# Performance work log

Hardware: AMD Instinct MI355X
Metric: run time of the kernel (lower is better)

## Reference

```python
import jax, jax.numpy as jnp
import numpy as np


def _maxpool2x2(t):
    # t: [B, C, H, W] -> [B, C, H//2, W//2]
    B, C, H, W = t.shape
    return t.reshape(B, C, H // 2, 2, W // 2, 2).max(axis=(3, 5))


def setup_inputs() -> dict:
    key = jax.random.key(0)
    ks = jax.random.split(key, 6)
    ch = 64
    B, H, W = 16, 64, 64
    x = jax.random.normal(ks[0], (B, ch, H, W), dtype=jnp.float32)
    # 1x1 conv weights (spectral-norm wrapper just rescales weights; use unit-scale weights)
    w_theta = jax.random.normal(ks[1], (ch // 8, ch), dtype=jnp.float32) * 0.05
    w_phi = jax.random.normal(ks[2], (ch // 8, ch), dtype=jnp.float32) * 0.05
    w_g = jax.random.normal(ks[3], (ch // 2, ch), dtype=jnp.float32) * 0.05
    w_o = jax.random.normal(ks[4], (ch, ch // 2), dtype=jnp.float32) * 0.05
    gamma = jnp.float32(0.5)  # nonzero so attention branch contributes
    return {"x": x, "w_theta": w_theta, "w_phi": w_phi, "w_g": w_g, "w_o": w_o, "gamma": gamma}


def reference(x, w_theta, w_phi, w_g, w_o, gamma):
    B, C, H, W = x.shape
    N = H * W
    # 1x1 convs are channel contractions
    theta = jnp.einsum('oc,bchw->bohw', w_theta, x).reshape(B, -1, N)          # [B, C/8, N]
    phi = _maxpool2x2(jnp.einsum('oc,bchw->bohw', w_phi, x)).reshape(B, -1, N // 4)  # [B, C/8, N/4]
    g = _maxpool2x2(jnp.einsum('oc,bchw->bohw', w_g, x)).reshape(B, -1, N // 4)      # [B, C/2, N/4]
    # attention: no scaling (faithful to source)
    scores = jnp.einsum('bdn,bdm->bnm', theta, phi)       # [B, N, N/4]
    beta = jax.nn.softmax(scores, axis=-1)
    o = jnp.einsum('bdm,bnm->bdn', g, beta)               # [B, C/2, N]
    o = o.reshape(B, C // 2, H, W)
    o = jnp.einsum('oc,bchw->bohw', w_o, o)               # [B, C, H, W]
    return gamma * o + x
```

## Files before the change

### kernel.cpp

```cpp
#include <hip/hip_runtime.h>
#include <hip/hip_bf16.h>

#define BB 16
#define CC 64
#define NN 4096
#define MM 1024

typedef unsigned short u16;
typedef __attribute__((ext_vector_type(8))) short bf16x8;
typedef __attribute__((ext_vector_type(4))) float f32x4;

__device__ inline u16 f2bf(float f) {
    union { float f; unsigned u; } v; v.f = f;
    return (u16)((v.u + 0x7FFFu + ((v.u >> 16) & 1u)) >> 16);
}
__device__ inline bf16x8 ld_bf16x8(const u16* p) {
    union { uint4 u; bf16x8 b; } c; c.u = *(const uint4*)p; return c.b;
}


__global__ __launch_bounds__(256) void prep_kernel(
    const float* __restrict__ x, const float* __restrict__ w_theta,
    const float* __restrict__ w_phi, const float* __restrict__ w_g,
    u16* __restrict__ theta_b, u16* __restrict__ phi_b, u16* __restrict__ gT_b)
{
    __shared__ float wT[64 * 48];
    __shared__ float pool[40 * 128];

    const int t = threadIdx.x;
    const int b = blockIdx.y;

    for (int i = t; i < 64 * 8; i += 256)  { int o = i >> 6, c = i & 63; wT[c * 48 + o] = w_theta[i]; }
    for (int i = t; i < 64 * 8; i += 256)  { int o = i >> 6, c = i & 63; wT[c * 48 + 8 + o] = w_phi[i]; }
    for (int i = t; i < 64 * 32; i += 256) { int o = i >> 6, c = i & 63; wT[c * 48 + 16 + o] = w_g[i]; }
    __syncthreads();

    const int p = blockIdx.x * 256 + t;
    const float* xb = x + (size_t)b * CC * NN;

    float xr[64];
    #pragma unroll
    for (int c = 0; c < 64; ++c) xr[c] = xb[c * NN + p];

    float4 acc[12];
    #pragma unroll
    for (int k = 0; k < 12; ++k) acc[k] = make_float4(0.f, 0.f, 0.f, 0.f);

    #pragma unroll
    for (int c = 0; c < 64; ++c) {
        const float xv = xr[c];
        const float4* w4 = (const float4*)&wT[c * 48];
        #pragma unroll
        for (int k = 0; k < 12; ++k) {
            float4 w = w4[k];
            acc[k].x += w.x * xv; acc[k].y += w.y * xv;
            acc[k].z += w.z * xv; acc[k].w += w.w * xv;
        }
    }

    {
        union { u16 s[8]; uint4 v; } tb;
        tb.s[0] = f2bf(acc[0].x); tb.s[1] = f2bf(acc[0].y);
        tb.s[2] = f2bf(acc[0].z); tb.s[3] = f2bf(acc[0].w);
        tb.s[4] = f2bf(acc[1].x); tb.s[5] = f2bf(acc[1].y);
        tb.s[6] = f2bf(acc[1].z); tb.s[7] = f2bf(acc[1].w);
        *(uint4*)(theta_b + ((size_t)b * NN + p) * 8) = tb.v;
    }

    const int col = t & 63, rp = t >> 6;
    float hm[40];
    #pragma unroll
    for (int k = 0; k < 10; ++k) {
        float4 a = acc[2 + k];
        hm[4 * k + 0] = a.x; hm[4 * k + 1] = a.y; hm[4 * k + 2] = a.z; hm[4 * k + 3] = a.w;
    }
    #pragma unroll
    for (int k = 0; k < 40; ++k) {
        float o = __shfl_xor(hm[k], 1, 64);
        hm[k] = fmaxf(hm[k], o);
    }
    if ((col & 1) == 0) {
        const int pc = col >> 1;
        #pragma unroll
        for (int k = 0; k < 40; ++k) pool[k * 128 + rp * 32 + pc] = hm[k];
    }
    __syncthreads();

    const int mrow0 = blockIdx.x * 2;
    for (int i = t; i < 2560; i += 256) {
        const int k = i >> 6, rem = i & 63, pr = rem >> 5, pcol = rem & 31;
        const float v = fmaxf(pool[k * 128 + (2 * pr) * 32 + pcol],
                              pool[k * 128 + (2 * pr + 1) * 32 + pcol]);
        const int m = (mrow0 + pr) * 32 + pcol;
        if (k < 8) phi_b[((size_t)b * MM + m) * 8 + k] = f2bf(v);
        else       gT_b[(size_t)b * 32 * MM + (size_t)(k - 8) * MM + m] = f2bf(v);
    }
}

__global__ __launch_bounds__(256) void attn_kernel(
    const u16* __restrict__ theta_b, const u16* __restrict__ phi_b,
    const u16* __restrict__ gT_b, float* __restrict__ o_ws)
{
    __shared__ u16 phis[64 * 8];
    __shared__ u16 gts[32 * 72];
    __shared__ u16 Ps[64 * 72];

    const int t = threadIdx.x;
    const int w = t >> 6, lane = t & 63;
    const int b = blockIdx.y, qbase = blockIdx.x * 64;
    const int m16 = lane & 15, quad = lane >> 4;

    bf16x8 thA = {0, 0, 0, 0, 0, 0, 0, 0};
    if (quad == 0)
        thA = ld_bf16x8(theta_b + ((size_t)b * NN + qbase + w * 16 + m16) * 8);

    bf16x8 onesB;
    #pragma unroll
    for (int i = 0; i < 8; ++i) onesB[i] = (short)0x3F80;

    const f32x4 zero4 = {0.f, 0.f, 0.f, 0.f};
    f32x4 oacc0 = zero4, oacc1 = zero4, lacc = zero4;

    const u16* phg = phi_b + (size_t)b * MM * 8;
    const u16* gtg = gT_b + (size_t)b * 32 * MM;

    for (int c = 0; c < 16; ++c) {
        __syncthreads();
        if (t < 64)
            *(uint4*)(phis + t * 8) = *(const uint4*)(phg + (size_t)(c * 64 + t) * 8);
        {
            const int d = t >> 3, part = t & 7;
            *(uint4*)(gts + d * 72 + part * 8) =
                *(const uint4*)(gtg + (size_t)d * MM + c * 64 + part * 8);
        }
        __syncthreads();

        f32x4 S[4];
        #pragma unroll
        for (int kc = 0; kc < 4; ++kc) {
            bf16x8 phB = {0, 0, 0, 0, 0, 0, 0, 0};
            if (quad == 0)
                phB = ld_bf16x8(phis + (kc * 16 + m16) * 8);
            S[kc] = __builtin_amdgcn_mfma_f32_16x16x32_bf16(thA, phB, zero4, 0, 0, 0);
        }

        #pragma unroll
        for (int kc = 0; kc < 4; ++kc) {
            #pragma unroll
            for (int r = 0; r < 4; ++r) {
                const float e = __expf(S[kc][r]);
                Ps[(w * 16 + quad * 4 + r) * 72 + kc * 16 + m16] = f2bf(e);
            }
        }

        #pragma unroll
        for (int kblk = 0; kblk < 2; ++kblk) {
            const bf16x8 pA = ld_bf16x8(Ps + (w * 16 + m16) * 72 + kblk * 32 + quad * 8);
            const bf16x8 g0 = ld_bf16x8(gts + m16 * 72 + kblk * 32 + quad * 8);
            const bf16x8 g1 = ld_bf16x8(gts + (16 + m16) * 72 + kblk * 32 + quad * 8);
            oacc0 = __builtin_amdgcn_mfma_f32_16x16x32_bf16(pA, g0, oacc0, 0, 0, 0);
            oacc1 = __builtin_amdgcn_mfma_f32_16x16x32_bf16(pA, g1, oacc1, 0, 0, 0);
            lacc  = __builtin_amdgcn_mfma_f32_16x16x32_bf16(pA, onesB, lacc, 0, 0, 0);
        }
    }

    float* dst = o_ws + ((size_t)b * NN + qbase + w * 16 + quad * 4) * 32 + m16;
    #pragma unroll
    for (int r = 0; r < 4; ++r) {
        const float inv = 1.0f / lacc[r];
        dst[r * 32]      = oacc0[r] * inv;
        dst[r * 32 + 16] = oacc1[r] * inv;
    }
}

__global__ __launch_bounds__(256) void out_kernel(
    const float* __restrict__ o_ws, const float* __restrict__ w_o,
    const float* __restrict__ x, const float* __restrict__ gamma_p,
    float* __restrict__ out)
{
    __shared__ float wos[64 * 32];
    const int t = threadIdx.x;
    for (int i = t; i < 2048; i += 256) wos[i] = w_o[i];
    __syncthreads();

    const int b = blockIdx.y;
    const int xid = blockIdx.x * 256 + t;
    const int half = xid >> 12;
    const int n = xid & 4095;
    const float gamma = *gamma_p;

    float4 ov[8];
    const float4* op = (const float4*)(o_ws + ((size_t)b * NN + n) * 32);
    #pragma unroll
    for (int d = 0; d < 8; ++d) ov[d] = op[d];

    const float* xb = x + (size_t)b * CC * NN;
    float* ob = out + (size_t)b * CC * NN;
    for (int ci = 0; ci < 32; ++ci) {
        const int c = half * 32 + ci;
        const float4* wr = (const float4*)(wos + c * 32);
        float acc = 0.f;
        #pragma unroll
        for (int d = 0; d < 8; ++d) {
            const float4 wv = wr[d];
            acc += wv.x * ov[d].x + wv.y * ov[d].y + wv.z * ov[d].z + wv.w * ov[d].w;
        }
        ob[c * NN + n] = gamma * acc + xb[c * NN + n];
    }
}

extern "C" void kernel_launch(void* const* d_in, const int* in_sizes, int n_in,
                              void* d_out, int out_size, void* d_ws, size_t ws_size,
                              hipStream_t stream) {
    const float* x       = (const float*)d_in[0];
    const float* w_theta = (const float*)d_in[1];
    const float* w_phi   = (const float*)d_in[2];
    const float* w_g     = (const float*)d_in[3];
    const float* w_o     = (const float*)d_in[4];
    const float* gamma   = (const float*)d_in[5];

    float* ws = (float*)d_ws;
    float* o_ws = ws;
    u16* theta_b = (u16*)(ws + 2097152);
    u16* phi_b   = theta_b + 524288;
    u16* gT_b    = phi_b + 131072;
    float* out   = (float*)d_out;

    prep_kernel<<<dim3(16, 16), 256, 0, stream>>>(x, w_theta, w_phi, w_g, theta_b, phi_b, gT_b);
    attn_kernel<<<dim3(64, 16), 256, 0, stream>>>(theta_b, phi_b, gT_b, o_ws);
    out_kernel<<<dim3(32, 16), 256, 0, stream>>>(o_ws, w_o, x, gamma, out);
}
```

Baseline: 137.1 us.

## Fuse attention with output projection and restructure prep kernel channel split

Merges the attention and output-projection kernels into one, computing the transposed attention output and applying w_o via an extra bf16 MFMA before the residual add, which removes the fp32 o_ws round trip through global memory and one launch. The prep kernel now splits output channels across waves with each thread handling four adjacent pixels, and does pooling with shuffles instead of a shared-memory pool buffer. The attention loop processes 128 keys per step, reads phi straight from global memory, and keeps the probabilities in registers instead of staging them through LDS. The output projection now runs in bf16, which loses some precision compared with the fp32 path.

```diff
diff --git a/kernel.cpp b/kernel.cpp
--- a/kernel.cpp
+++ b/kernel.cpp
@@ -1,5 +1,4 @@
 #include <hip/hip_runtime.h>
-#include <hip/hip_bf16.h>
 
 #define BB 16
 #define CC 64
@@ -7,15 +6,25 @@
 #define MM 1024
 
 typedef unsigned short u16;
+typedef unsigned int u32;
 typedef __attribute__((ext_vector_type(8))) short bf16x8;
 typedef __attribute__((ext_vector_type(4))) float f32x4;
 
 __device__ inline u16 f2bf(float f) {
-    union { float f; unsigned u; } v; v.f = f;
+    union { float f; u32 u; } v; v.f = f;
     return (u16)((v.u + 0x7FFFu + ((v.u >> 16) & 1u)) >> 16);
 }
 __device__ inline bf16x8 ld_bf16x8(const u16* p) {
     union { uint4 u; bf16x8 b; } c; c.u = *(const uint4*)p; return c.b;
+}
+__device__ inline bf16x8 ld2_bf16x8(const u16* p0, const u16* p1) {
+    union { uint2 u[2]; bf16x8 b; } c;
+    c.u[0] = *(const uint2*)p0;
+    c.u[1] = *(const uint2*)p1;
+    return c.b;
+}
+__device__ inline uint2 pack4(u16 a, u16 b, u16 c, u16 d) {
+    uint2 r; r.x = (u32)a | ((u32)b << 16); r.y = (u32)c | ((u32)d << 16); return r;
 }
 
 
@@ -25,9 +34,8 @@
     u16* __restrict__ theta_b, u16* __restrict__ phi_b, u16* __restrict__ gT_b)
 {
     __shared__ float wT[64 * 48];
-    __shared__ float pool[40 * 128];
-
-    const int t = threadIdx.x;
+
+    const int t = threadIdx.x, w = t >> 6, l = t & 63;
     const int b = blockIdx.y;
 
     for (int i = t; i < 64 * 8; i += 256)  { int o = i >> 6, c = i & 63; wT[c * 48 + o] = w_theta[i]; }
@@ -35,177 +43,166 @@
     for (int i = t; i < 64 * 32; i += 256) { int o = i >> 6, c = i & 63; wT[c * 48 + 16 + o] = w_g[i]; }
     __syncthreads();
 
-    const int p = blockIdx.x * 256 + t;
-    const float* xb = x + (size_t)b * CC * NN;
-
-    float xr[64];
-    #pragma unroll
-    for (int c = 0; c < 64; ++c) xr[c] = xb[c * NN + p];
-
-    float4 acc[12];
-    #pragma unroll
-    for (int k = 0; k < 12; ++k) acc[k] = make_float4(0.f, 0.f, 0.f, 0.f);
-
-    #pragma unroll
+    const int nbase = blockIdx.x * 256;
+    const float* xb = x + (size_t)b * CC * NN + nbase + 4 * l;
+
+    float acc[12][4];
+    #pragma unroll
+    for (int k = 0; k < 12; ++k)
+        #pragma unroll
+        for (int p = 0; p < 4; ++p) acc[k][p] = 0.f;
+
+    #pragma unroll 4
     for (int c = 0; c < 64; ++c) {
-        const float xv = xr[c];
-        const float4* w4 = (const float4*)&wT[c * 48];
+        const float4 xv = *(const float4*)(xb + c * NN);
+        const float4* wp = (const float4*)(wT + c * 48 + w * 12);
+        const float4 wa = wp[0], wb = wp[1], wc = wp[2];
+        const float wk[12] = {wa.x, wa.y, wa.z, wa.w, wb.x, wb.y, wb.z, wb.w,
+                              wc.x, wc.y, wc.z, wc.w};
         #pragma unroll
         for (int k = 0; k < 12; ++k) {
-            float4 w = w4[k];
-            acc[k].x += w.x * xv; acc[k].y += w.y * xv;
-            acc[k].z += w.z * xv; acc[k].w += w.w * xv;
-        }
-    }
-
-    {
-        union { u16 s[8]; uint4 v; } tb;
-        tb.s[0] = f2bf(acc[0].x); tb.s[1] = f2bf(acc[0].y);
-        tb.s[2] = f2bf(acc[0].z); tb.s[3] = f2bf(acc[0].w);
-        tb.s[4] = f2bf(acc[1].x); tb.s[5] = f2bf(acc[1].y);
-        tb.s[6] = f2bf(acc[1].z); tb.s[7] = f2bf(acc[1].w);
-        *(uint4*)(theta_b + ((size_t)b * NN + p) * 8) = tb.v;
-    }
-
-    const int col = t & 63, rp = t >> 6;
-    float hm[40];
-    #pragma unroll
-    for (int k = 0; k < 10; ++k) {
-        float4 a = acc[2 + k];
-        hm[4 * k + 0] = a.x; hm[4 * k + 1] = a.y; hm[4 * k + 2] = a.z; hm[4 * k + 3] = a.w;
-    }
-    #pragma unroll
-    for (int k = 0; k < 40; ++k) {
-        float o = __shfl_xor(hm[k], 1, 64);
-        hm[k] = fmaxf(hm[k], o);
-    }
-    if ((col & 1) == 0) {
-        const int pc = col >> 1;
-        #pragma unroll
-        for (int k = 0; k < 40; ++k) pool[k * 128 + rp * 32 + pc] = hm[k];
-    }
-    __syncthreads();
-
-    const int mrow0 = blockIdx.x * 2;
-    for (int i = t; i < 2560; i += 256) {
-        const int k = i >> 6, rem = i & 63, pr = rem >> 5, pcol = rem & 31;
-        const float v = fmaxf(pool[k * 128 + (2 * pr) * 32 + pcol],
-                              pool[k * 128 + (2 * pr + 1) * 32 + pcol]);
-        const int m = (mrow0 + pr) * 32 + pcol;
-        if (k < 8) phi_b[((size_t)b * MM + m) * 8 + k] = f2bf(v);
-        else       gT_b[(size_t)b * 32 * MM + (size_t)(k - 8) * MM + m] = f2bf(v);
-    }
-}
-
-__global__ __launch_bounds__(256) void attn_kernel(
+            acc[k][0] += wk[k] * xv.x; acc[k][1] += wk[k] * xv.y;
+            acc[k][2] += wk[k] * xv.z; acc[k][3] += wk[k] * xv.w;
+        }
+    }
+
+    if (w == 0) {
+        #pragma unroll
+        for (int p = 0; p < 4; ++p) {
+            union { u16 s[8]; uint4 v; } tb;
+            #pragma unroll
+            for (int k = 0; k < 8; ++k) tb.s[k] = f2bf(acc[k][p]);
+            *(uint4*)(theta_b + ((size_t)b * NN + nbase + 4 * l + p) * 8) = tb.v;
+        }
+    }
+
+    const int start = (w == 0) ? 8 : 0;
+    float v0[12], v1[12];
+    #pragma unroll
+    for (int k = 0; k < 12; ++k) {
+        if (k < start) continue;
+        float h0 = fmaxf(acc[k][0], acc[k][1]);
+        float h1 = fmaxf(acc[k][2], acc[k][3]);
+        v0[k] = fmaxf(h0, __shfl_xor(h0, 16, 64));
+        v1[k] = fmaxf(h1, __shfl_xor(h1, 16, 64));
+    }
+    if ((l & 16) == 0) {
+        const int prow = l >> 5;
+        const int m = (blockIdx.x * 2 + prow) * 32 + 2 * (l & 15);
+        #pragma unroll
+        for (int k = 0; k < 12; ++k) {
+            if (k < start) continue;
+            const int kg = w * 12 + k;
+            if (kg < 16) {
+                phi_b[((size_t)b * MM + m) * 8 + (kg - 8)]     = f2bf(v0[k]);
+                phi_b[((size_t)b * MM + m + 1) * 8 + (kg - 8)] = f2bf(v1[k]);
+            } else {
+                *(u32*)(gT_b + (size_t)b * 32 * MM + (size_t)(kg - 16) * MM + m) =
+                    (u32)f2bf(v0[k]) | ((u32)f2bf(v1[k]) << 16);
+            }
+        }
+    }
+}
+
+__global__ __launch_bounds__(256, 4) void attn_out_kernel(
     const u16* __restrict__ theta_b, const u16* __restrict__ phi_b,
-    const u16* __restrict__ gT_b, float* __restrict__ o_ws)
-{
-    __shared__ u16 phis[64 * 8];
-    __shared__ u16 gts[32 * 72];
-    __shared__ u16 Ps[64 * 72];
-
-    const int t = threadIdx.x;
-    const int w = t >> 6, lane = t & 63;
-    const int b = blockIdx.y, qbase = blockIdx.x * 64;
-    const int m16 = lane & 15, quad = lane >> 4;
-
-    bf16x8 thA = {0, 0, 0, 0, 0, 0, 0, 0};
-    if (quad == 0)
-        thA = ld_bf16x8(theta_b + ((size_t)b * NN + qbase + w * 16 + m16) * 8);
-
-    bf16x8 onesB;
-    #pragma unroll
-    for (int i = 0; i < 8; ++i) onesB[i] = (short)0x3F80;
-
-    const f32x4 zero4 = {0.f, 0.f, 0.f, 0.f};
-    f32x4 oacc0 = zero4, oacc1 = zero4, lacc = zero4;
-
-    const u16* phg = phi_b + (size_t)b * MM * 8;
-    const u16* gtg = gT_b + (size_t)b * 32 * MM;
-
-    for (int c = 0; c < 16; ++c) {
-        __syncthreads();
-        if (t < 64)
-            *(uint4*)(phis + t * 8) = *(const uint4*)(phg + (size_t)(c * 64 + t) * 8);
-        {
-            const int d = t >> 3, part = t & 7;
-            *(uint4*)(gts + d * 72 + part * 8) =
-                *(const uint4*)(gtg + (size_t)d * MM + c * 64 + part * 8);
-        }
-        __syncthreads();
-
-        f32x4 S[4];
-        #pragma unroll
-        for (int kc = 0; kc < 4; ++kc) {
-            bf16x8 phB = {0, 0, 0, 0, 0, 0, 0, 0};
-            if (quad == 0)
-                phB = ld_bf16x8(phis + (kc * 16 + m16) * 8);
-            S[kc] = __builtin_amdgcn_mfma_f32_16x16x32_bf16(thA, phB, zero4, 0, 0, 0);
-        }
-
-        #pragma unroll
-        for (int kc = 0; kc < 4; ++kc) {
-            #pragma unroll
-            for (int r = 0; r < 4; ++r) {
-                const float e = __expf(S[kc][r]);
-                Ps[(w * 16 + quad * 4 + r) * 72 + kc * 16 + m16] = f2bf(e);
-            }
-        }
-
-        #pragma unroll
-        for (int kblk = 0; kblk < 2; ++kblk) {
-            const bf16x8 pA = ld_bf16x8(Ps + (w * 16 + m16) * 72 + kblk * 32 + quad * 8);
-            const bf16x8 g0 = ld_bf16x8(gts + m16 * 72 + kblk * 32 + quad * 8);
-            const bf16x8 g1 = ld_bf16x8(gts + (16 + m16) * 72 + kblk * 32 + quad * 8);
-            oacc0 = __builtin_amdgcn_mfma_f32_16x16x32_bf16(pA, g0, oacc0, 0, 0, 0);
-            oacc1 = __builtin_amdgcn_mfma_f32_16x16x32_bf16(pA, g1, oacc1, 0, 0, 0);
-            lacc  = __builtin_amdgcn_mfma_f32_16x16x32_bf16(pA, onesB, lacc, 0, 0, 0);
-        }
-    }
-
-    float* dst = o_ws + ((size_t)b * NN + qbase + w * 16 + quad * 4) * 32 + m16;
-    #pragma unroll
-    for (int r = 0; r < 4; ++r) {
-        const float inv = 1.0f / lacc[r];
-        dst[r * 32]      = oacc0[r] * inv;
-        dst[r * 32 + 16] = oacc1[r] * inv;
-    }
-}
-
-__global__ __launch_bounds__(256) void out_kernel(
-    const float* __restrict__ o_ws, const float* __restrict__ w_o,
+    const u16* __restrict__ gT_b, const float* __restrict__ w_o,
     const float* __restrict__ x, const float* __restrict__ gamma_p,
     float* __restrict__ out)
 {
-    __shared__ float wos[64 * 32];
-    const int t = threadIdx.x;
-    for (int i = t; i < 2048; i += 256) wos[i] = w_o[i];
+    __shared__ u16 gs[32 * 136];
+    __shared__ u16 oS[64 * 40];
+
+    const int t = threadIdx.x, w = t >> 6, lane = t & 63;
+    const int m16 = lane & 15, quad = lane >> 4;
+    const int b = blockIdx.y, qbase = blockIdx.x * 64;
+
+    bf16x8 thB = {0, 0, 0, 0, 0, 0, 0, 0};
+    if (quad == 0)
+        thB = ld_bf16x8(theta_b + ((size_t)b * NN + qbase + w * 16 + m16) * 8);
+
+    bf16x8 woA[4];
+    #pragma unroll
+    for (int cf = 0; cf < 4; ++cf) {
+        const float* wp = w_o + (cf * 16 + m16) * 32 + quad * 8;
+        const float4 f0 = *(const float4*)wp;
+        const float4 f1 = *(const float4*)(wp + 4);
+        bf16x8 a;
+        a[0] = f2bf(f0.x); a[1] = f2bf(f0.y); a[2] = f2bf(f0.z); a[3] = f2bf(f0.w);
+        a[4] = f2bf(f1.x); a[5] = f2bf(f1.y); a[6] = f2bf(f1.z); a[7] = f2bf(f1.w);
+        woA[cf] = a;
+    }
+
+    bf16x8 onesA;
+    #pragma unroll
+    for (int i = 0; i < 8; ++i) onesA[i] = (short)0x3F80;
+
+    const f32x4 zero4 = {0.f, 0.f, 0.f, 0.f};
+    f32x4 oT0 = zero4, oT1 = zero4, lacc = zero4;
+
+    const u16* phg = phi_b + (size_t)b * MM * 8;
+    const u16* gtg = gT_b + (size_t)b * 32 * MM;
+
+    for (int it = 0; it < 8; ++it) {
+        const int keybase = it * 128;
+        __syncthreads();
+        #pragma unroll
+        for (int p2 = 0; p2 < 2; ++p2) {
+            const int d = p2 * 16 + (t >> 4);
+            const int k0 = (t & 15) * 8;
+            *(uint4*)(gs + d * 136 + k0) =
+                *(const uint4*)(gtg + (size_t)d * MM + keybase + k0);
+        }
+        __syncthreads();
+
+        #pragma unroll
+        for (int kblk = 0; kblk < 4; ++kblk) {
+            bf16x8 phA0 = {0, 0, 0, 0, 0, 0, 0, 0};
+            bf16x8 phA1 = {0, 0, 0, 0, 0, 0, 0, 0};
+            if (quad == 0) {
+                phA0 = ld_bf16x8(phg + (size_t)(keybase + kblk * 32 + m16) * 8);
+                phA1 = ld_bf16x8(phg + (size_t)(keybase + kblk * 32 + 16 + m16) * 8);
+            }
+            const f32x4 Sa = __builtin_amdgcn_mfma_f32_16x16x32_bf16(phA0, thB, zero4, 0, 0, 0);
+            const f32x4 Sb = __builtin_amdgcn_mfma_f32_16x16x32_bf16(phA1, thB, zero4, 0, 0, 0);
+
+            bf16x8 pB;
+            #pragma unroll
+            for (int r = 0; r < 4; ++r) {
+                pB[r]     = (short)f2bf(__expf(Sa[r]));
+                pB[4 + r] = (short)f2bf(__expf(Sb[r]));
+            }
+
+            const u16* g0p = gs + m16 * 136 + kblk * 32 + quad * 4;
+            const u16* g1p = gs + (16 + m16) * 136 + kblk * 32 + quad * 4;
+            const bf16x8 gA0 = ld2_bf16x8(g0p, g0p + 16);
+            const bf16x8 gA1 = ld2_bf16x8(g1p, g1p + 16);
+
+            oT0  = __builtin_amdgcn_mfma_f32_16x16x32_bf16(gA0, pB, oT0, 0, 0, 0);
+            oT1  = __builtin_amdgcn_mfma_f32_16x16x32_bf16(gA1, pB, oT1, 0, 0, 0);
+            lacc = __builtin_amdgcn_mfma_f32_16x16x32_bf16(onesA, pB, lacc, 0, 0, 0);
+        }
+    }
+
+    const float inv = 1.0f / lacc[0];
+    u16* orow = oS + (w * 16 + m16) * 40;
+    *(uint2*)(orow + quad * 4) =
+        pack4(f2bf(oT0[0] * inv), f2bf(oT0[1] * inv), f2bf(oT0[2] * inv), f2bf(oT0[3] * inv));
+    *(uint2*)(orow + 16 + quad * 4) =
+        pack4(f2bf(oT1[0] * inv), f2bf(oT1[1] * inv), f2bf(oT1[2] * inv), f2bf(oT1[3] * inv));
     __syncthreads();
 
-    const int b = blockIdx.y;
-    const int xid = blockIdx.x * 256 + t;
-    const int half = xid >> 12;
-    const int n = xid & 4095;
+    const bf16x8 oB = ld_bf16x8(oS + (w * 16 + m16) * 40 + quad * 8);
     const float gamma = *gamma_p;
-
-    float4 ov[8];
-    const float4* op = (const float4*)(o_ws + ((size_t)b * NN + n) * 32);
-    #pragma unroll
-    for (int d = 0; d < 8; ++d) ov[d] = op[d];
-
-    const float* xb = x + (size_t)b * CC * NN;
-    float* ob = out + (size_t)b * CC * NN;
-    for (int ci = 0; ci < 32; ++ci) {
-        const int c = half * 32 + ci;
-        const float4* wr = (const float4*)(wos + c * 32);
-        float acc = 0.f;
-        #pragma unroll
-        for (int d = 0; d < 8; ++d) {
-            const float4 wv = wr[d];
-            acc += wv.x * ov[d].x + wv.y * ov[d].y + wv.z * ov[d].z + wv.w * ov[d].w;
-        }
-        ob[c * NN + n] = gamma * acc + xb[c * NN + n];
+    #pragma unroll
+    for (int cf = 0; cf < 4; ++cf) {
+        const f32x4 D = __builtin_amdgcn_mfma_f32_16x16x32_bf16(woA[cf], oB, zero4, 0, 0, 0);
+        #pragma unroll
+        for (int r = 0; r < 4; ++r) {
+            const int c = cf * 16 + quad * 4 + r;
+            const size_t adr = ((size_t)b * CC + c) * NN + qbase + w * 16 + m16;
+            out[adr] = gamma * D[r] + x[adr];
+        }
     }
 }
 
@@ -219,14 +216,13 @@
     const float* w_o     = (const float*)d_in[4];
     const float* gamma   = (const float*)d_in[5];
 
-    float* ws = (float*)d_ws;
-    float* o_ws = ws;
-    u16* theta_b = (u16*)(ws + 2097152);
+    u16* theta_b = (u16*)d_ws;
     u16* phi_b   = theta_b + 524288;
     u16* gT_b    = phi_b + 131072;
     float* out   = (float*)d_out;
 
-    prep_kernel<<<dim3(16, 16), 256, 0, stream>>>(x, w_theta, w_phi, w_g, theta_b, phi_b, gT_b);
-    attn_kernel<<<dim3(64, 16), 256, 0, stream>>>(theta_b, phi_b, gT_b, o_ws);
-    out_kernel<<<dim3(32, 16), 256, 0, stream>>>(o_ws, w_o, x, gamma, out);
-}
+    prep_kernel<<<dim3(16, 16), 256, 0, stream>>>(x, w_theta, w_phi, w_g,
+                                                  theta_b, phi_b, gT_b);
+    attn_out_kernel<<<dim3(64, 16), 256, 0, stream>>>(theta_b, phi_b, gT_b,
+                                                      w_o, x, gamma, out);
+}
```

Measured after the change: 120.2 us. 12.3% less time.
